# Kernel tuning notes

Hardware: AMD Instinct MI355X
Metric: run time of the kernel (lower is better)

The kernel has to match this reference:

```python
import jax, jax.numpy as jnp
import numpy as np

LN_EPS = 1e-5
NEG_SLOPE = 0.01  # torch LeakyReLU default
H, D = 16, 64


def _layernorm(x, g, b):
    m = jnp.mean(x, axis=-1, keepdims=True)
    v = jnp.var(x, axis=-1, keepdims=True)
    return (x - m) * jax.lax.rsqrt(v + LN_EPS) * g + b


def _mlp(x, ln_g, ln_b, W1, b1, W2, b2):
    h = _layernorm(x, ln_g, ln_b)
    h = jax.nn.gelu(h @ W1 + b1, approximate=False)
    return h @ W2 + b2


def _gather_nodes(node_msg, edge_index):
    # node_msg: (b,n,c), edge_index: (b,n,k) -> (b,n,k,c)
    return jax.vmap(lambda nm, ei: nm[ei])(node_msg, edge_index)


def setup_inputs() -> dict:
    key = jax.random.key(0)
    ks = jax.random.split(key, 16)
    b, n, k = 2, 1024, 32
    dim, pdim, msg_dim = 512, 256, 256
    s = 0.02
    inp = {
        'node_repr': jax.random.normal(ks[0], (b, n, dim), jnp.float32),
        'edge_repr': jax.random.normal(ks[1], (b, n, k, pdim), jnp.float32),
        'edge_index': jax.random.randint(ks[2], (b, n, k), 0, n, jnp.int32),
        'edge_mask': jax.random.randint(ks[3], (b, n, k), 0, 2, jnp.int32),
        'mask_bw': jnp.ones((b, n, k, 1), jnp.float32),
        'W_edge_msg': s * jax.random.normal(ks[4], (pdim, msg_dim), jnp.float32),
        'W_node_src': s * jax.random.normal(ks[5], (dim, msg_dim), jnp.float32),
        'W_node_tgt': s * jax.random.normal(ks[6], (dim, msg_dim), jnp.float32),
        'msg_ln_g': jnp.ones((msg_dim,), jnp.float32),
        'msg_ln_b': jnp.zeros((msg_dim,), jnp.float32),
        'msg_W1': s * jax.random.normal(ks[7], (msg_dim, 4 * msg_dim), jnp.float32),
        'msg_b1': jnp.zeros((4 * msg_dim,), jnp.float32),
        'msg_W2': s * jax.random.normal(ks[8], (4 * msg_dim, msg_dim), jnp.float32),
        'msg_b2': jnp.zeros((msg_dim,), jnp.float32),
        'W_gate': jnp.zeros((dim, msg_dim), jnp.float32),   # init_weights: zeros
        'b_gate': -jnp.ones((msg_dim,), jnp.float32),       # init_weights: -1
        'W_out': s * jax.random.normal(ks[9], (msg_dim, dim), jnp.float32),
        'W_msg': s * jax.random.normal(ks[10], (msg_dim, msg_dim), jnp.float32),
        'W_attn_bias': s * jax.random.normal(ks[11], (msg_dim, H), jnp.float32),
        'W_gat_value': s * jax.random.normal(ks[12], (msg_dim, H * D), jnp.float32),
        'W_gat_gate': jnp.zeros((dim, H * D), jnp.float32),
        'b_gat_gate': -jnp.ones((H * D,), jnp.float32),
        'W_gat_out': s * jax.random.normal(ks[13], (H * D, dim), jnp.float32),
        'node_ln_g': jnp.ones((dim,), jnp.float32),
        'node_ln_b': jnp.zeros((dim,), jnp.float32),
        'node_W1': s * jax.random.normal(ks[14], (dim, 4 * dim), jnp.float32),
        'node_b1': jnp.zeros((4 * dim,), jnp.float32),
        'node_W2': s * jax.random.normal(ks[15], (4 * dim, dim), jnp.float32),
        'node_b2': jnp.zeros((dim,), jnp.float32),
    }
    return inp


def reference(node_repr, edge_repr, edge_index, edge_mask, mask_bw,
              W_edge_msg, W_node_src, W_node_tgt,
              msg_ln_g, msg_ln_b, msg_W1, msg_b1, msg_W2, msg_b2,
              W_gate, b_gate, W_out,
              W_msg, W_attn_bias, W_gat_value, W_gat_gate, b_gat_gate, W_gat_out,
              node_ln_g, node_ln_b, node_W1, node_b1, node_W2, node_b2):
    b, n, k = edge_index.shape
    em_bool = edge_mask.astype(bool)          # (b,n,k)
    em_f = edge_mask.astype(node_repr.dtype)

    # edge-wise message: edge proj + gathered src node proj + broadcast tgt node proj
    node_msg = node_repr @ W_node_src                      # (b,n,msg)
    msg = edge_repr @ W_edge_msg \
        + _gather_nodes(node_msg, edge_index) * mask_bw \
        + (node_repr @ W_node_tgt)[:, :, None, :]          # (b,n,k,msg)
    msg = _mlp(msg, msg_ln_g, msg_ln_b, msg_W1, msg_b1, msg_W2, msg_b2)
    msg = jnp.where(em_bool[..., None], msg, 0.0)

    # global (mean-pooled, gated) path
    o = (msg * em_f[..., None]).sum(-2) / (em_f.sum(-1, keepdims=True) + 1e-6)
    o = jax.nn.sigmoid(node_repr @ W_gate + b_gate) * o
    dh = o @ W_out                                         # (b,n,dim)

    # GAT path: per-node attention over its k neighbors
    ab = jnp.where(NEG_SLOPE < 1, jax.nn.leaky_relu(msg @ W_msg, NEG_SLOPE), msg) @ W_attn_bias  # (b,n,k,H)
    ab = jnp.where(em_bool[..., None], ab, -jnp.finfo(ab.dtype).max)
    attn = jax.nn.softmax(ab, axis=2)                      # softmax over k
    v = (msg @ W_gat_value).reshape(b, n, k, H, D)
    og = jnp.einsum('bnkh,bnkhd->bnhd', attn, v).reshape(b, n, H * D)
    og = jax.nn.sigmoid(node_repr @ W_gat_gate + b_gat_gate) * og
    dh = dh + og @ W_gat_out

    # residual + node MLP (dropout is identity in eval mode)
    node_repr = node_repr + dh
    node_repr = node_repr + _mlp(node_repr, node_ln_g, node_ln_b, node_W1, node_b1, node_W2, node_b2)
    return node_repr
```

## Files before the change

kernel.cpp:

```cpp
#include <hip/hip_runtime.h>
#include <hip/hip_bf16.h>

typedef unsigned short u16;
typedef short s16x8 __attribute__((ext_vector_type(8)));
typedef float f32x4 __attribute__((ext_vector_type(4)));
typedef float f32x8 __attribute__((ext_vector_type(8)));
typedef u16 u16x8 __attribute__((ext_vector_type(8)));

#define DEV static __device__ __forceinline__

DEV float b2f(u16 u){ unsigned int i=((unsigned int)u)<<16; float f; __builtin_memcpy(&f,&i,4); return f; }
DEV u16 f2b(float x){ __hip_bfloat16 h=__float2bfloat16(x); u16 u; __builtin_memcpy(&u,&h,2); return u; }
DEV f32x4 MFMA(s16x8 a, s16x8 b, f32x4 c){ return __builtin_amdgcn_mfma_f32_16x16x32_bf16(a,b,c,0,0,0); }
DEV s16x8 LD8(const u16* p){ return *(const s16x8*)p; }
DEV s16x8 cvt8(const float* p){
  s16x8 r;
  #pragma unroll
  for (int i=0;i<8;i++) r[i] = (short)f2b(p[i]);
  return r;
}
DEV float geluf(float x){ return 0.5f*x*(1.0f+erff(x*0.70710678118654752f)); }
DEV float sigmf(float x){ return 1.0f/(1.0f+__expf(-x)); }

DEV void gload16(const u16* g, u16* l){
  __builtin_amdgcn_global_load_lds((const __attribute__((address_space(1))) void*)g,
                                   (__attribute__((address_space(3))) void*)l, 16, 0, 0);
}

#define WS_WeT   0
#define WS_W1T   65536
#define WS_W2T   327680
#define WS_WmT   589824
#define WS_WvT   655360
#define WS_WoT   917504
#define WS_WgoT  1048576
#define WS_nW1T  1572864
#define WS_nW2T  2621440
#define WS_SrcT  3670016
#define WS_TgtT  3801088
#define WS_GateT 3932160
#define WS_GgT   4063232
#define WS_NM    4587520
#define WS_TGT   5111808
#define WS_GP    5636096
#define WS_GG    6160384
#define WS_MSG   8257536
#define WS_U2    8257536
#define WS_X     10354688
#define WS_Y     12451840
#define WS_WM    25034752
#define WS_U1    33423360
#define WS_YE    33947648
#define WS_H     50724864

struct P13 { const float* p[13]; };
__device__ const int TR_START[14] = {0,16,80,144,160,224,256,384,640,896,928,960,992,1120};
__device__ const int TR_R[13]   = {256,256,1024,256,256,256,1024,512,2048,512,512,512,512};
__device__ const int TR_C[13]   = {256,1024,256,256,1024,512,512,2048,512,256,256,256,1024};
__device__ const int TR_DST[13] = {WS_WeT,WS_W1T,WS_W2T,WS_WmT,WS_WvT,WS_WoT,WS_WgoT,
                                   WS_nW1T,WS_nW2T,WS_SrcT,WS_TgtT,WS_GateT,WS_GgT};

__global__ __launch_bounds__(256) void k_transpose(P13 ps, u16* __restrict__ ws){
  __shared__ alignas(16) u16 Ts[64][72];
  const int t = threadIdx.x;
  int bid = blockIdx.x;
  int mi = 0;
  #pragma unroll 1
  while (bid >= TR_START[mi+1]) ++mi;
  const float* src = ps.p[mi];
  const int R = TR_R[mi], C = TR_C[mi];
  u16* dst = ws + TR_DST[mi];
  const int ti = bid - TR_START[mi];
  const int tcn = C >> 6;
  const int tr = ti / tcn, tc = ti % tcn;
  {
    const int row = t >> 2, cs = (t & 3) * 16;
    const float* sp = src + (tr*64 + row)*C + tc*64 + cs;
    u16x8 a, b;
    #pragma unroll
    for (int i=0;i<8;i++){ a[i]=f2b(sp[i]); b[i]=f2b(sp[8+i]); }
    *(u16x8*)&Ts[row][cs]   = a;
    *(u16x8*)&Ts[row][cs+8] = b;
  }
  __syncthreads();
  {
    const int col = t >> 2, rs = (t & 3) * 16;
    u16x8 a, b;
    #pragma unroll
    for (int i=0;i<8;i++){ a[i]=Ts[rs+i][col]; b[i]=Ts[rs+8+i][col]; }
    u16* dp = dst + (tc*64 + col)*R + tr*64 + rs;
    *(u16x8*)dp = a;
    *(u16x8*)(dp+8) = b;
  }
}

__global__ __launch_bounds__(256) void k_proj(const float* __restrict__ node_repr,
                                              const float* __restrict__ bgate,
                                              const float* __restrict__ bgg,
                                              u16* __restrict__ ws){
  const int t=threadIdx.x, lid=t&63, w=t>>6, g=lid>>4, q=lid&15;
  const int rb = blockIdx.x, yb = blockIdx.y;
  const u16* BT; u16* dst; int Nseg, colbase, act=0; const float* bias=nullptr;
  if (yb < 4){ BT=ws+WS_SrcT;  dst=ws+WS_NM; Nseg=256;  colbase=yb*64; }
  else if (yb < 8){ BT=ws+WS_TgtT;  dst=ws+WS_TGT; Nseg=256; colbase=(yb-4)*64; }
  else if (yb < 12){ BT=ws+WS_GateT; dst=ws+WS_GP; Nseg=256; colbase=(yb-8)*64; act=1; bias=bgate; }
  else { BT=ws+WS_GgT; dst=ws+WS_GG; Nseg=1024; colbase=(yb-12)*64; act=1; bias=bgg; }
  const int wr=(w>>1)*32, wcl=(w&1)*32;
  f32x4 acc[2][2] = {};
  for (int kk=0; kk<512; kk+=32){
    s16x8 af[2], bfr[2];
    #pragma unroll
    for (int i=0;i<2;i++) af[i] = cvt8(node_repr + (rb*64 + wr + i*16 + q)*512 + kk + 8*g);
    #pragma unroll
    for (int j=0;j<2;j++) bfr[j] = LD8(BT + (colbase + wcl + j*16 + q)*512 + kk + 8*g);
    #pragma unroll
    for (int i=0;i<2;i++)
      #pragma unroll
      for (int j=0;j<2;j++) acc[i][j] = MFMA(af[i], bfr[j], acc[i][j]);
  }
  #pragma unroll
  for (int i=0;i<2;i++)
    #pragma unroll
    for (int j=0;j<2;j++)
      #pragma unroll
      for (int r=0;r<4;r++){
        const int row = rb*64 + wr + i*16 + g*4 + r;
        const int col = wcl + j*16 + q;
        float v = acc[i][j][r];
        if (act) v = sigmf(v + bias[colbase+col]);
        dst[row*Nseg + colbase + col] = f2b(v);
      }
}

#define GB_S 528
__global__ __launch_bounds__(256) void k_edgepre(
    const float* __restrict__ edge_repr, const int* __restrict__ edge_index,
    const float* __restrict__ mask_bw,
    const float* __restrict__ ln_g, const float* __restrict__ ln_b,
    u16* __restrict__ ws)
{
  __shared__ alignas(16) char Gb[64*GB_S];
  __shared__ alignas(16) u16 As[64*32];
  __shared__ alignas(16) u16 Bs[256*32];
  __shared__ float rsS[4][64], rsQ[4][64];
  __shared__ int idxL[64]; __shared__ float mbwL[64];

  const int t=threadIdx.x, lid=t&63, w=t>>6, g=lid>>4, q=lid&15;
  const int R0 = blockIdx.x * 64;
  const int wc = w * 64;

  if (t < 64){
    idxL[t] = edge_index[R0+t];
    mbwL[t] = mask_bw[R0+t];
  }
  __syncthreads();

  const u16* nm = ws + WS_NM;
  const u16* tg = ws + WS_TGT;

  #pragma unroll
  for (int it=0; it<8; ++it){
    const int v = t + 256*it;
    const int row = v >> 5;
    const int sc  = (v & 31) * 8;
    const int er  = R0 + row;
    const int gnd = er >> 5;
    const int bi  = gnd >> 10;
    const int srow = bi*1024 + idxL[row];
    const float mb = mbwL[row];
    u16x8 nv = *(const u16x8*)(nm + srow*256 + sc);
    u16x8 tv = *(const u16x8*)(tg + gnd*256 + sc);
    u16x8 ov;
    #pragma unroll
    for (int j2=0;j2<8;j2++) ov[j2] = f2b(b2f(nv[j2])*mb + b2f(tv[j2]));
    *(u16x8*)(Gb + row*GB_S + 2*sc) = ov;
  }
  __syncthreads();

  f32x4 acc[4][4];
  #pragma unroll
  for (int i=0;i<4;i++)
    #pragma unroll
    for (int r=0;r<4;r++){
      const int row = i*16 + g*4 + r;
      #pragma unroll
      for (int j=0;j<4;j++){
        const int col = wc + j*16 + q;
        acc[i][j][r] = b2f(*(const u16*)(Gb + row*GB_S + 2*col));
      }
    }
  for (int kk=0; kk<256; kk+=32){
    __syncthreads();
    {
      const int row = t >> 2, c0 = (t & 3) * 8;
      const float* sp = edge_repr + (R0 + row)*256 + kk + c0;
      u16x8 av;
      #pragma unroll
      for (int j2=0;j2<8;j2++) av[j2] = f2b(sp[j2]);
      *(u16x8*)(As + row*32 + c0) = av;
    }
    #pragma unroll
    for (int j=0;j<4;j++){
      const int s = t + 256*j;
      const int brow = s >> 2, ko = (s & 3) * 8;
      u16* ldsB = Bs + (w*64 + 256*j)*8;
      gload16(ws + WS_WeT + brow*256 + kk + ko, ldsB);
    }
    __syncthreads();
    s16x8 af[4], bfr[4];
    #pragma unroll
    for (int i=0;i<4;i++) af[i]  = *(const s16x8*)(As + (i*16+q)*32 + g*8);
    #pragma unroll
    for (int j=0;j<4;j++) bfr[j] = *(const s16x8*)(Bs + (wc + j*16 + q)*32 + g*8);
    #pragma unroll
    for (int i=0;i<4;i++)
      #pragma unroll
      for (int j=0;j<4;j++) acc[i][j] = MFMA(af[i], bfr[j], acc[i][j]);
  }
  #pragma unroll
  for (int i=0;i<4;i++)
    #pragma unroll
    for (int r=0;r<4;r++){
      float s=0.f, s2=0.f;
      #pragma unroll
      for (int j=0;j<4;j++){ float v=acc[i][j][r]; s+=v; s2+=v*v; }
      #pragma unroll
      for (int m=1;m<16;m<<=1){ s += __shfl_xor(s,m,64); s2 += __shfl_xor(s2,m,64); }
      if (q==0){ const int row=i*16+g*4+r; rsS[w][row]=s; rsQ[w][row]=s2; }
    }
  __syncthreads();
  u16* Ye = ws + WS_YE;
  #pragma unroll
  for (int i=0;i<4;i++)
    #pragma unroll
    for (int r=0;r<4;r++){
      const int row=i*16+g*4+r;
      const float s  = rsS[0][row]+rsS[1][row]+rsS[2][row]+rsS[3][row];
      const float s2 = rsQ[0][row]+rsQ[1][row]+rsQ[2][row]+rsQ[3][row];
      const float mean = s*(1.f/256.f);
      const float var  = s2*(1.f/256.f) - mean*mean;
      const float rstd = rsqrtf(var + 1e-5f);
      #pragma unroll
      for (int j=0;j<4;j++){
        const int col = wc + j*16 + q;
        Ye[(R0+row)*256 + col] = f2b((acc[i][j][r]-mean)*rstd*ln_g[col] + ln_b[col]);
      }
    }
}

__global__ __launch_bounds__(256) void k_mlp1(const u16* __restrict__ A,
                                              const u16* __restrict__ BT,
                                              const float* __restrict__ b1,
                                              u16* __restrict__ H){
  __shared__ alignas(16) u16 As[128*32];
  __shared__ alignas(16) u16 Bs[128*32];
  const int t=threadIdx.x, lid=t&63, w=t>>6, g=lid>>4, q=lid&15;
  const int r0 = blockIdx.x*128, n0 = blockIdx.y*128;
  const int wr=(w>>1)*64, wc2=(w&1)*64;
  f32x4 acc[4][4] = {};
  for (int kk=0;kk<256;kk+=32){
    __syncthreads();
    #pragma unroll
    for (int j=0;j<2;j++){
      const int v = t + 256*j;
      const int row = v>>2, sg = (v&3)*8;
      u16* ldsA = As + (w*64 + 256*j)*8;
      u16* ldsB = Bs + (w*64 + 256*j)*8;
      gload16(A  + (r0+row)*256 + kk + sg, ldsA);
      gload16(BT + (n0+row)*256 + kk + sg, ldsB);
    }
    __syncthreads();
    s16x8 af[4], bf_[4];
    #pragma unroll
    for (int i=0;i<4;i++) af[i]  = *(const s16x8*)(As + (wr+i*16+q)*32 + g*8);
    #pragma unroll
    for (int j=0;j<4;j++) bf_[j] = *(const s16x8*)(Bs + (wc2+j*16+q)*32 + g*8);
    #pragma unroll
    for (int i=0;i<4;i++)
      #pragma unroll
      for (int j=0;j<4;j++) acc[i][j] = MFMA(af[i], bf_[j], acc[i][j]);
  }
  #pragma unroll
  for (int i=0;i<4;i++)
    #pragma unroll
    for (int j=0;j<4;j++)
      #pragma unroll
      for (int r=0;r<4;r++){
        const int row = r0 + wr + i*16 + g*4 + r;
        const int col = n0 + wc2 + j*16 + q;
        H[row*1024 + col] = f2b(geluf(acc[i][j][r] + b1[col]));
      }
}

__global__ __launch_bounds__(256) void k_mlp2(const u16* __restrict__ A,
                                              const u16* __restrict__ BT,
                                              const float* __restrict__ b2,
                                              const int* __restrict__ em,
                                              u16* __restrict__ msg){
  __shared__ alignas(16) u16 As[128*32];
  __shared__ alignas(16) u16 Bs[128*32];
  __shared__ int emL[128];
  const int t=threadIdx.x, lid=t&63, w=t>>6, g=lid>>4, q=lid&15;
  const int r0 = blockIdx.x*128, n0 = blockIdx.y*128;
  const int wr=(w>>1)*64, wc2=(w&1)*64;
  if (t < 128) emL[t] = em[r0 + t];
  f32x4 acc[4][4] = {};
  for (int kk=0;kk<1024;kk+=32){
    __syncthreads();
    #pragma unroll
    for (int j=0;j<2;j++){
      const int v = t + 256*j;
      const int row = v>>2, sg = (v&3)*8;
      u16* ldsA = As + (w*64 + 256*j)*8;
      u16* ldsB = Bs + (w*64 + 256*j)*8;
      gload16(A  + (r0+row)*1024 + kk + sg, ldsA);
      gload16(BT + (n0+row)*1024 + kk + sg, ldsB);
    }
    __syncthreads();
    s16x8 af[4], bf_[4];
    #pragma unroll
    for (int i=0;i<4;i++) af[i]  = *(const s16x8*)(As + (wr+i*16+q)*32 + g*8);
    #pragma unroll
    for (int j=0;j<4;j++) bf_[j] = *(const s16x8*)(Bs + (wc2+j*16+q)*32 + g*8);
    #pragma unroll
    for (int i=0;i<4;i++)
      #pragma unroll
      for (int j=0;j<4;j++) acc[i][j] = MFMA(af[i], bf_[j], acc[i][j]);
  }
  #pragma unroll
  for (int i=0;i<4;i++)
    #pragma unroll
    for (int j=0;j<4;j++)
      #pragma unroll
      for (int r=0;r<4;r++){
        const int rl  = wr + i*16 + g*4 + r;
        const int col = n0 + wc2 + j*16 + q;
        float v = acc[i][j][r] + b2[col];
        if (!emL[rl]) v = 0.f;
        msg[(r0+rl)*256 + col] = f2b(v);
      }
}

__global__ __launch_bounds__(256) void k_tm(const u16* __restrict__ A,
                                            const u16* __restrict__ BT,
                                            u16* __restrict__ Tm){
  __shared__ alignas(16) u16 As[128*32];
  __shared__ alignas(16) u16 Bs[128*32];
  const int t=threadIdx.x, lid=t&63, w=t>>6, g=lid>>4, q=lid&15;
  const int r0 = blockIdx.x*128, n0 = blockIdx.y*128;
  const int wr=(w>>1)*64, wc2=(w&1)*64;
  f32x4 acc[4][4] = {};
  for (int kk=0;kk<256;kk+=32){
    __syncthreads();
    #pragma unroll
    for (int j=0;j<2;j++){
      const int v = t + 256*j;
      const int row = v>>2, sg = (v&3)*8;
      u16* ldsA = As + (w*64 + 256*j)*8;
      u16* ldsB = Bs + (w*64 + 256*j)*8;
      gload16(A  + (r0+row)*256 + kk + sg, ldsA);
      gload16(BT + (n0+row)*256 + kk + sg, ldsB);
    }
    __syncthreads();
    s16x8 af[4], bf_[4];
    #pragma unroll
    for (int i=0;i<4;i++) af[i]  = *(const s16x8*)(As + (wr+i*16+q)*32 + g*8);
    #pragma unroll
    for (int j=0;j<4;j++) bf_[j] = *(const s16x8*)(Bs + (wc2+j*16+q)*32 + g*8);
    #pragma unroll
    for (int i=0;i<4;i++)
      #pragma unroll
      for (int j=0;j<4;j++) acc[i][j] = MFMA(af[i], bf_[j], acc[i][j]);
  }
  #pragma unroll
  for (int i=0;i<4;i++)
    #pragma unroll
    for (int j=0;j<4;j++)
      #pragma unroll
      for (int r=0;r<4;r++){
        const int row = r0 + wr + i*16 + g*4 + r;
        const int col = n0 + wc2 + j*16 + q;
        float v = acc[i][j][r];
        Tm[row*256 + col] = f2b(v > 0.f ? v : 0.01f*v);
      }
}

__global__ __launch_bounds__(256) void k_ab(const u16* __restrict__ A,
                                            const float* __restrict__ Wab,
                                            float* __restrict__ AB){
  __shared__ alignas(16) u16 As[128*32];
  __shared__ alignas(16) char WbT[16*528];
  const int t=threadIdx.x, lid=t&63, w=t>>6, g=lid>>4, q=lid&15;
  const int r0 = blockIdx.x*128;
  {
    const float* wr_ = Wab + t*16;
    #pragma unroll
    for (int h=0;h<16;h++) *(u16*)(WbT + h*528 + 2*t) = f2b(wr_[h]);
  }
  f32x4 acc[2] = {};
  for (int kk=0;kk<256;kk+=32){
    __syncthreads();
    #pragma unroll
    for (int j=0;j<2;j++){
      const int s = t + 256*j;
      const int row = s>>2, ko = (s&3)*8;
      u16* ldsA = As + (w*64 + 256*j)*8;
      gload16(A + (r0+row)*256 + kk + ko, ldsA);
    }
    __syncthreads();
    s16x8 bf_ = *(const s16x8*)(WbT + q*528 + 2*(kk + 8*g));
    #pragma unroll
    for (int i=0;i<2;i++){
      s16x8 af = *(const s16x8*)(As + (w*32 + i*16 + q)*32 + g*8);
      acc[i] = MFMA(af, bf_, acc[i]);
    }
  }
  #pragma unroll
  for (int i=0;i<2;i++)
    #pragma unroll
    for (int r=0;r<4;r++){
      const int row = r0 + w*32 + i*16 + g*4 + r;
      AB[row*16 + q] = acc[i][r];
    }
}

#define AM_S 528
#define MT_S 80
__global__ __launch_bounds__(256) void k_attn2(const int* __restrict__ edge_mask,
                                               u16* __restrict__ ws){
  __shared__ alignas(16) char Am[32*AM_S];
  __shared__ alignas(16) char Mt[256*MT_S];
  __shared__ alignas(16) char Pb[16*80];
  __shared__ float Pp[32][16];
  __shared__ int emL[32];
  __shared__ float cntS;

  const int t=threadIdx.x, lid=t&63, w=t>>6, g=lid>>4, q=lid&15;
  const int nd = blockIdx.x;
  const int wc = w*64;
  const u16* msg = ws + WS_MSG + nd*32*256;
  const float* ab = (const float*)(ws + WS_YE) + nd*32*16;

  if (t < 32) emL[t] = edge_mask[nd*32 + t];
  #pragma unroll
  for (int it=0; it<4; ++it){
    const int v = t + 256*it;
    const int row = v >> 5, sc = (v & 31)*8;
    u16x8 val = *(const u16x8*)(msg + row*256 + sc);
    *(u16x8*)(Am + row*AM_S + 2*sc) = val;
  }
  {
    const int k = t >> 4, h = t & 15;
    Pp[k][h]    = ab[k*16 + h];
    Pp[k+16][h] = ab[(k+16)*16 + h];
  }
  __syncthreads();
  if (t == 0){ float c=0.f; for (int k=0;k<32;k++) c += emL[k]?1.f:0.f; cntS=c; }
  {
    const int c = t;
    #pragma unroll 1
    for (int k=0;k<32;k++){
      u16 vv = *(const u16*)(Am + k*AM_S + 2*c);
      *(u16*)(Mt + c*MT_S + 2*k) = vv;
    }
  }
  if (t < 16){
    const int h = t;
    float m = -3.4028235e38f;
    float pv[32];
    for (int k=0;k<32;k++){ pv[k] = emL[k] ? Pp[k][h] : -3.4028235e38f; m = fmaxf(m, pv[k]); }
    float s = 0.f;
    float ev[32];
    for (int k=0;k<32;k++){ ev[k]=__expf(pv[k]-m); s+=ev[k]; }
    const float inv = 1.f/s;
    for (int k=0;k<32;k++) *(u16*)(Pb + h*80 + 2*k) = f2b(ev[k]*inv);
  }
  __syncthreads();
  {
    s16x8 pa = *(const s16x8*)(Pb + q*80 + 2*(8*g));
    f32x4 wmac[4] = {};
    #pragma unroll
    for (int j=0;j<4;j++){
      s16x8 mb = *(const s16x8*)(Mt + (wc + j*16 + q)*MT_S + 2*(8*g));
      wmac[j] = MFMA(pa, mb, wmac[j]);
    }
    u16* wmw = ws + WS_WM;
    #pragma unroll
    for (int j=0;j<4;j++)
      #pragma unroll
      for (int r=0;r<4;r++){
        const int hh = g*4 + r;
        const int col = wc + j*16 + q;
        wmw[hh*(2048*256) + nd*256 + col] = f2b(wmac[j][r]);
      }
  }
  {
    const int c = t;
    float s = 0.f;
    #pragma unroll 1
    for (int k=0;k<32;k++) s += b2f(*(const u16*)(Am + k*AM_S + 2*c));
    const float o = s / (cntS + 1e-6f);
    ws[WS_U1 + nd*256 + c] = f2b(o * b2f(ws[WS_GP + nd*256 + c]));
  }
}

__global__ __launch_bounds__(256) void k_og(u16* __restrict__ ws){
  const int t=threadIdx.x, lid=t&63, w=t>>6, g=lid>>4, q=lid&15;
  const int rb=blockIdx.x, h=blockIdx.y;
  const int wr=(w>>1)*32, wcl=(w&1)*32;
  const u16* A  = ws + WS_WM  + h*(2048*256);
  const u16* BT = ws + WS_WvT;
  f32x4 acc[2][2] = {};
  for (int kk=0;kk<256;kk+=32){
    s16x8 af[2], bfr[2];
    #pragma unroll
    for (int i=0;i<2;i++) af[i] = LD8(A + (rb*64 + wr + i*16 + q)*256 + kk + 8*g);
    #pragma unroll
    for (int j=0;j<2;j++) bfr[j] = LD8(BT + (h*64 + wcl + j*16 + q)*256 + kk + 8*g);
    #pragma unroll
    for (int i=0;i<2;i++)
      #pragma unroll
      for (int j=0;j<2;j++) acc[i][j] = MFMA(af[i], bfr[j], acc[i][j]);
  }
  #pragma unroll
  for (int i=0;i<2;i++)
    #pragma unroll
    for (int j=0;j<2;j++)
      #pragma unroll
      for (int r=0;r<4;r++){
        const int row = rb*64 + wr + i*16 + g*4 + r;
        const int col = h*64 + wcl + j*16 + q;
        const float gv = b2f(ws[WS_GG + row*1024 + col]);
        ws[WS_U2 + row*1024 + col] = f2b(acc[i][j][r] * gv);
      }
}

__global__ __launch_bounds__(256) void k_dh(const float* __restrict__ node_repr, u16* __restrict__ ws){
  const int t=threadIdx.x, lid=t&63, w=t>>6, g=lid>>4, q=lid&15;
  const int rb=blockIdx.x, cb=blockIdx.y*64;
  const int wr=(w>>1)*32, wcl=(w&1)*32;
  float* Xf = (float*)(ws + WS_X);
  f32x4 acc[2][2] = {};
  for (int kk=0;kk<256;kk+=32){
    s16x8 af[2], bfr[2];
    #pragma unroll
    for (int i=0;i<2;i++) af[i] = LD8(ws + WS_U1 + (rb*64 + wr + i*16 + q)*256 + kk + 8*g);
    #pragma unroll
    for (int j=0;j<2;j++) bfr[j] = LD8(ws + WS_WoT + (cb + wcl + j*16 + q)*256 + kk + 8*g);
    #pragma unroll
    for (int i=0;i<2;i++)
      #pragma unroll
      for (int j=0;j<2;j++) acc[i][j] = MFMA(af[i], bfr[j], acc[i][j]);
  }
  for (int kk=0;kk<1024;kk+=32){
    s16x8 af[2], bfr[2];
    #pragma unroll
    for (int i=0;i<2;i++) af[i] = LD8(ws + WS_U2 + (rb*64 + wr + i*16 + q)*1024 + kk + 8*g);
    #pragma unroll
    for (int j=0;j<2;j++) bfr[j] = LD8(ws + WS_WgoT + (cb + wcl + j*16 + q)*1024 + kk + 8*g);
    #pragma unroll
    for (int i=0;i<2;i++)
      #pragma unroll
      for (int j=0;j<2;j++) acc[i][j] = MFMA(af[i], bfr[j], acc[i][j]);
  }
  #pragma unroll
  for (int i=0;i<2;i++)
    #pragma unroll
    for (int j=0;j<2;j++)
      #pragma unroll
      for (int r=0;r<4;r++){
        const int row = rb*64 + wr + i*16 + g*4 + r;
        const int col = cb + wcl + j*16 + q;
        Xf[row*512 + col] = acc[i][j][r] + node_repr[row*512 + col];
      }
}

__global__ __launch_bounds__(256) void k_ln512(const float* __restrict__ g_, const float* __restrict__ b_,
                                               u16* __restrict__ ws){
  const int t=threadIdx.x, wid=t>>6, lane=t&63;
  const int row = blockIdx.x*4 + wid;
  const float* xr = (const float*)(ws + WS_X) + row*512;
  f32x8 xv = *(const f32x8*)(xr + lane*8);
  float s=0.f, s2=0.f;
  #pragma unroll
  for (int i=0;i<8;i++){ s+=xv[i]; s2+=xv[i]*xv[i]; }
  #pragma unroll
  for (int m=1;m<64;m<<=1){ s += __shfl_xor(s,m,64); s2 += __shfl_xor(s2,m,64); }
  const float mean = s*(1.f/512.f);
  const float var  = s2*(1.f/512.f) - mean*mean;
  const float rstd = rsqrtf(var + 1e-5f);
  u16x8 yv;
  #pragma unroll
  for (int i=0;i<8;i++) yv[i] = f2b((xv[i]-mean)*rstd*g_[lane*8+i] + b_[lane*8+i]);
  *(u16x8*)(ws + WS_Y + row*512 + lane*8) = yv;
}

__global__ __launch_bounds__(256) void k_nmlp1(const u16* __restrict__ A,
                                               const u16* __restrict__ BT,
                                               const float* __restrict__ b1,
                                               u16* __restrict__ H){
  __shared__ alignas(16) u16 As[128*32];
  __shared__ alignas(16) u16 Bs[128*32];
  const int t=threadIdx.x, lid=t&63, w=t>>6, g=lid>>4, q=lid&15;
  const int r0 = blockIdx.x*128, n0 = blockIdx.y*128;
  const int wr=(w>>1)*64, wc2=(w&1)*64;
  f32x4 acc[4][4] = {};
  for (int kk=0;kk<512;kk+=32){
    __syncthreads();
    #pragma unroll
    for (int j=0;j<2;j++){
      const int v = t + 256*j;
      const int row = v>>2, sg = (v&3)*8;
      u16* ldsA = As + (w*64 + 256*j)*8;
      u16* ldsB = Bs + (w*64 + 256*j)*8;
      gload16(A  + (r0+row)*512 + kk + sg, ldsA);
      gload16(BT + (n0+row)*512 + kk + sg, ldsB);
    }
    __syncthreads();
    s16x8 af[4], bf_[4];
    #pragma unroll
    for (int i=0;i<4;i++) af[i]  = *(const s16x8*)(As + (wr+i*16+q)*32 + g*8);
    #pragma unroll
    for (int j=0;j<4;j++) bf_[j] = *(const s16x8*)(Bs + (wc2+j*16+q)*32 + g*8);
    #pragma unroll
    for (int i=0;i<4;i++)
      #pragma unroll
      for (int j=0;j<4;j++) acc[i][j] = MFMA(af[i], bf_[j], acc[i][j]);
  }
  #pragma unroll
  for (int i=0;i<4;i++)
    #pragma unroll
    for (int j=0;j<4;j++)
      #pragma unroll
      for (int r=0;r<4;r++){
        const int row = r0 + wr + i*16 + g*4 + r;
        const int col = n0 + wc2 + j*16 + q;
        H[row*2048 + col] = f2b(geluf(acc[i][j][r] + b1[col]));
      }
}

__global__ __launch_bounds__(256) void k_nmlp2(const u16* __restrict__ A,
                                               const u16* __restrict__ BT,
                                               const float* __restrict__ b2,
                                               const float* __restrict__ Xf,
                                               float* __restrict__ out){
  __shared__ alignas(16) u16 As[64*32];
  __shared__ alignas(16) u16 Bs[64*32];
  const int t=threadIdx.x, lid=t&63, w=t>>6, g=lid>>4, q=lid&15;
  const int r0 = blockIdx.x*64, n0 = blockIdx.y*64;
  const int wr=(w>>1)*32, wc2=(w&1)*32;
  f32x4 acc[2][2] = {};
  for (int kk=0;kk<2048;kk+=32){
    __syncthreads();
    {
      const int row = t>>2, sg = (t&3)*8;
      u16* ldsA = As + (w*64)*8;
      u16* ldsB = Bs + (w*64)*8;
      gload16(A  + (r0+row)*2048 + kk + sg, ldsA);
      gload16(BT + (n0+row)*2048 + kk + sg, ldsB);
    }
    __syncthreads();
    s16x8 af[2], bf_[2];
    #pragma unroll
    for (int i=0;i<2;i++) af[i]  = *(const s16x8*)(As + (wr+i*16+q)*32 + g*8);
    #pragma unroll
    for (int j=0;j<2;j++) bf_[j] = *(const s16x8*)(Bs + (wc2+j*16+q)*32 + g*8);
    #pragma unroll
    for (int i=0;i<2;i++)
      #pragma unroll
      for (int j=0;j<2;j++) acc[i][j] = MFMA(af[i], bf_[j], acc[i][j]);
  }
  #pragma unroll
  for (int i=0;i<2;i++)
    #pragma unroll
    for (int j=0;j<2;j++)
      #pragma unroll
      for (int r=0;r<4;r++){
        const int row = r0 + wr + i*16 + g*4 + r;
        const int col = n0 + wc2 + j*16 + q;
        out[row*512 + col] = acc[i][j][r] + b2[col] + Xf[row*512 + col];
      }
}

extern "C" void kernel_launch(void* const* d_in, const int* in_sizes, int n_in,
                              void* d_out, int out_size, void* d_ws, size_t ws_size,
                              hipStream_t stream){
  (void)in_sizes; (void)n_in; (void)out_size; (void)ws_size;
  const float* node_repr = (const float*)d_in[0];
  const float* edge_repr = (const float*)d_in[1];
  const int* edge_index = (const int*)d_in[2];
  const int* edge_mask  = (const int*)d_in[3];
  const float* mask_bw = (const float*)d_in[4];
  u16* ws = (u16*)d_ws;

  P13 ps;
  const int srcIdx[13] = {5,10,12,17,19,16,22,25,27,6,7,14,20};
  for (int i=0;i<13;i++) ps.p[i] = (const float*)d_in[srcIdx[i]];

  hipLaunchKernelGGL(k_transpose, dim3(1120), dim3(256), 0, stream, ps, ws);
  hipLaunchKernelGGL(k_proj, dim3(32,28), dim3(256), 0, stream,
                     node_repr, (const float*)d_in[15], (const float*)d_in[21], ws);
  hipLaunchKernelGGL(k_edgepre, dim3(1024), dim3(256), 0, stream,
                     edge_repr, edge_index, mask_bw,
                     (const float*)d_in[8], (const float*)d_in[9], ws);
  for (int grp=0; grp<2; ++grp){
    const u16* Ag = ws + WS_YE + grp*32768*256;
    u16* Hg = ws + WS_H;
    u16* msgg = ws + WS_MSG + grp*32768*256;
    const int* emg = edge_mask + grp*32768;
    hipLaunchKernelGGL(k_mlp1, dim3(256,8), dim3(256), 0, stream,
                       Ag, ws + WS_W1T, (const float*)d_in[11], Hg);
    hipLaunchKernelGGL(k_mlp2, dim3(256,2), dim3(256), 0, stream,
                       Hg, ws + WS_W2T, (const float*)d_in[13], emg, msgg);
  }
  hipLaunchKernelGGL(k_tm, dim3(512,2), dim3(256), 0, stream,
                     ws + WS_MSG, ws + WS_WmT, ws + WS_H);
  hipLaunchKernelGGL(k_ab, dim3(512), dim3(256), 0, stream,
                     ws + WS_H, (const float*)d_in[18], (float*)(ws + WS_YE));
  hipLaunchKernelGGL(k_attn2, dim3(2048), dim3(256), 0, stream,
                     edge_mask, ws);
  hipLaunchKernelGGL(k_og, dim3(32,16), dim3(256), 0, stream, ws);
  hipLaunchKernelGGL(k_dh, dim3(32,8), dim3(256), 0, stream, node_repr, ws);
  hipLaunchKernelGGL(k_ln512, dim3(512), dim3(256), 0, stream,
                     (const float*)d_in[23], (const float*)d_in[24], ws);
  hipLaunchKernelGGL(k_nmlp1, dim3(16,16), dim3(256), 0, stream,
                     ws + WS_Y, ws + WS_nW1T, (const float*)d_in[26], ws + WS_H);
  hipLaunchKernelGGL(k_nmlp2, dim3(32,8), dim3(256), 0, stream,
                     ws + WS_H, ws + WS_nW2T, (const float*)d_in[28],
                     (const float*)(ws + WS_X), (float*)d_out);
}
```

Before: 357.4 us.

## Use tanh GELU, alias LDS in edge prologue, stage k_dh operands through LDS

Replaces the exact erf-based GELU in both MLP first-layer epilogues with a tanh approximation built on __expf, cutting transcendental cost. In k_edgepre the edge GEMM now runs first and the gathered node term is added afterwards, which lets the gather buffer and the A/B tiles share one LDS allocation and lowers LDS use, possibly raising occupancy. k_dh now stages its A and B tiles through LDS with global_load_lds instead of reading them directly from global memory per lane. The tanh GELU is an approximation that deviates slightly from the reference's exact GELU.

```diff
diff --git a/kernel.cpp b/kernel.cpp
--- a/kernel.cpp
+++ b/kernel.cpp
@@ -19,7 +19,12 @@
   for (int i=0;i<8;i++) r[i] = (short)f2b(p[i]);
   return r;
 }
-DEV float geluf(float x){ return 0.5f*x*(1.0f+erff(x*0.70710678118654752f)); }
+DEV float gelu_fast(float x){
+  float u = 0.7978845608f*(x + 0.044715f*x*x*x);
+  float e = __expf(2.f*u);
+  float th = 1.f - 2.f/(e + 1.f);
+  return 0.5f*x*(1.f + th);
+}
 DEV float sigmf(float x){ return 1.0f/(1.0f+__expf(-x)); }
 
 DEV void gload16(const u16* g, u16* l){
@@ -139,25 +144,54 @@
     const float* __restrict__ ln_g, const float* __restrict__ ln_b,
     u16* __restrict__ ws)
 {
-  __shared__ alignas(16) char Gb[64*GB_S];
-  __shared__ alignas(16) u16 As[64*32];
-  __shared__ alignas(16) u16 Bs[256*32];
+  __shared__ alignas(16) char SH[64*GB_S];
   __shared__ float rsS[4][64], rsQ[4][64];
   __shared__ int idxL[64]; __shared__ float mbwL[64];
 
   const int t=threadIdx.x, lid=t&63, w=t>>6, g=lid>>4, q=lid&15;
   const int R0 = blockIdx.x * 64;
   const int wc = w * 64;
+  u16* As = (u16*)SH;
+  u16* Bs = (u16*)(SH + 4096);
 
   if (t < 64){
     idxL[t] = edge_index[R0+t];
     mbwL[t] = mask_bw[R0+t];
   }
+
+  f32x4 acc[4][4] = {};
+  for (int kk=0; kk<256; kk+=32){
+    __syncthreads();
+    {
+      const int row = t >> 2, c0 = (t & 3) * 8;
+      const float* sp = edge_repr + (R0 + row)*256 + kk + c0;
+      u16x8 av;
+      #pragma unroll
+      for (int j2=0;j2<8;j2++) av[j2] = f2b(sp[j2]);
+      *(u16x8*)(As + row*32 + c0) = av;
+    }
+    #pragma unroll
+    for (int j=0;j<4;j++){
+      const int s = t + 256*j;
+      const int brow = s >> 2, ko = (s & 3) * 8;
+      u16* ldsB = Bs + (w*64 + 256*j)*8;
+      gload16(ws + WS_WeT + brow*256 + kk + ko, ldsB);
+    }
+    __syncthreads();
+    s16x8 af[4], bfr[4];
+    #pragma unroll
+    for (int i=0;i<4;i++) af[i]  = *(const s16x8*)(As + (i*16+q)*32 + g*8);
+    #pragma unroll
+    for (int j=0;j<4;j++) bfr[j] = *(const s16x8*)(Bs + (wc + j*16 + q)*32 + g*8);
+    #pragma unroll
+    for (int i=0;i<4;i++)
+      #pragma unroll
+      for (int j=0;j<4;j++) acc[i][j] = MFMA(af[i], bfr[j], acc[i][j]);
+  }
   __syncthreads();
 
   const u16* nm = ws + WS_NM;
   const u16* tg = ws + WS_TGT;
-
   #pragma unroll
   for (int it=0; it<8; ++it){
     const int v = t + 256*it;
@@ -173,11 +207,9 @@
     u16x8 ov;
     #pragma unroll
     for (int j2=0;j2<8;j2++) ov[j2] = f2b(b2f(nv[j2])*mb + b2f(tv[j2]));
-    *(u16x8*)(Gb + row*GB_S + 2*sc) = ov;
+    *(u16x8*)(SH + row*GB_S + 2*sc) = ov;
   }
   __syncthreads();
-
-  f32x4 acc[4][4];
   #pragma unroll
   for (int i=0;i<4;i++)
     #pragma unroll
@@ -186,37 +218,9 @@
       #pragma unroll
       for (int j=0;j<4;j++){
         const int col = wc + j*16 + q;
-        acc[i][j][r] = b2f(*(const u16*)(Gb + row*GB_S + 2*col));
-      }
-    }
-  for (int kk=0; kk<256; kk+=32){
-    __syncthreads();
-    {
-      const int row = t >> 2, c0 = (t & 3) * 8;
-      const float* sp = edge_repr + (R0 + row)*256 + kk + c0;
-      u16x8 av;
-      #pragma unroll
-      for (int j2=0;j2<8;j2++) av[j2] = f2b(sp[j2]);
-      *(u16x8*)(As + row*32 + c0) = av;
-    }
-    #pragma unroll
-    for (int j=0;j<4;j++){
-      const int s = t + 256*j;
-      const int brow = s >> 2, ko = (s & 3) * 8;
-      u16* ldsB = Bs + (w*64 + 256*j)*8;
-      gload16(ws + WS_WeT + brow*256 + kk + ko, ldsB);
-    }
-    __syncthreads();
-    s16x8 af[4], bfr[4];
-    #pragma unroll
-    for (int i=0;i<4;i++) af[i]  = *(const s16x8*)(As + (i*16+q)*32 + g*8);
-    #pragma unroll
-    for (int j=0;j<4;j++) bfr[j] = *(const s16x8*)(Bs + (wc + j*16 + q)*32 + g*8);
-    #pragma unroll
-    for (int i=0;i<4;i++)
-      #pragma unroll
-      for (int j=0;j<4;j++) acc[i][j] = MFMA(af[i], bfr[j], acc[i][j]);
-  }
+        acc[i][j][r] += b2f(*(const u16*)(SH + row*GB_S + 2*col));
+      }
+    }
   #pragma unroll
   for (int i=0;i<4;i++)
     #pragma unroll
@@ -288,7 +292,7 @@
       for (int r=0;r<4;r++){
         const int row = r0 + wr + i*16 + g*4 + r;
         const int col = n0 + wc2 + j*16 + q;
-        H[row*1024 + col] = f2b(geluf(acc[i][j][r] + b1[col]));
+        H[row*1024 + col] = f2b(gelu_fast(acc[i][j][r] + b1[col]));
       }
 }
 
@@ -536,32 +540,48 @@
 }
 
 __global__ __launch_bounds__(256) void k_dh(const float* __restrict__ node_repr, u16* __restrict__ ws){
+  __shared__ alignas(16) u16 As[64*32];
+  __shared__ alignas(16) u16 Bs[64*32];
   const int t=threadIdx.x, lid=t&63, w=t>>6, g=lid>>4, q=lid&15;
   const int rb=blockIdx.x, cb=blockIdx.y*64;
-  const int wr=(w>>1)*32, wcl=(w&1)*32;
+  const int wr=(w>>1)*32, wc2=(w&1)*32;
   float* Xf = (float*)(ws + WS_X);
   f32x4 acc[2][2] = {};
   for (int kk=0;kk<256;kk+=32){
-    s16x8 af[2], bfr[2];
-    #pragma unroll
-    for (int i=0;i<2;i++) af[i] = LD8(ws + WS_U1 + (rb*64 + wr + i*16 + q)*256 + kk + 8*g);
-    #pragma unroll
-    for (int j=0;j<2;j++) bfr[j] = LD8(ws + WS_WoT + (cb + wcl + j*16 + q)*256 + kk + 8*g);
+    __syncthreads();
+    {
+      const int row = t>>2, sg = (t&3)*8;
+      gload16(ws + WS_U1  + (rb*64+row)*256 + kk + sg, As + (w*64)*8);
+      gload16(ws + WS_WoT + (cb+row)*256    + kk + sg, Bs + (w*64)*8);
+    }
+    __syncthreads();
+    s16x8 af[2], bf_[2];
+    #pragma unroll
+    for (int i=0;i<2;i++) af[i]  = *(const s16x8*)(As + (wr+i*16+q)*32 + g*8);
+    #pragma unroll
+    for (int j=0;j<2;j++) bf_[j] = *(const s16x8*)(Bs + (wc2+j*16+q)*32 + g*8);
     #pragma unroll
     for (int i=0;i<2;i++)
       #pragma unroll
-      for (int j=0;j<2;j++) acc[i][j] = MFMA(af[i], bfr[j], acc[i][j]);
+      for (int j=0;j<2;j++) acc[i][j] = MFMA(af[i], bf_[j], acc[i][j]);
   }
   for (int kk=0;kk<1024;kk+=32){
-    s16x8 af[2], bfr[2];
-    #pragma unroll
-    for (int i=0;i<2;i++) af[i] = LD8(ws + WS_U2 + (rb*64 + wr + i*16 + q)*1024 + kk + 8*g);
-    #pragma unroll
-    for (int j=0;j<2;j++) bfr[j] = LD8(ws + WS_WgoT + (cb + wcl + j*16 + q)*1024 + kk + 8*g);
+    __syncthreads();
+    {
+      const int row = t>>2, sg = (t&3)*8;
+      gload16(ws + WS_U2   + (rb*64+row)*1024 + kk + sg, As + (w*64)*8);
+      gload16(ws + WS_WgoT + (cb+row)*1024    + kk + sg, Bs + (w*64)*8);
+    }
+    __syncthreads();
+    s16x8 af[2], bf_[2];
+    #pragma unroll
+    for (int i=0;i<2;i++) af[i]  = *(const s16x8*)(As + (wr+i*16+q)*32 + g*8);
+    #pragma unroll
+    for (int j=0;j<2;j++) bf_[j] = *(const s16x8*)(Bs + (wc2+j*16+q)*32 + g*8);
     #pragma unroll
     for (int i=0;i<2;i++)
       #pragma unroll
-      for (int j=0;j<2;j++) acc[i][j] = MFMA(af[i], bfr[j], acc[i][j]);
+      for (int j=0;j<2;j++) acc[i][j] = MFMA(af[i], bf_[j], acc[i][j]);
   }
   #pragma unroll
   for (int i=0;i<2;i++)
@@ -570,7 +590,7 @@
       #pragma unroll
       for (int r=0;r<4;r++){
         const int row = rb*64 + wr + i*16 + g*4 + r;
-        const int col = cb + wcl + j*16 + q;
+        const int col = cb + wc2 + j*16 + q;
         Xf[row*512 + col] = acc[i][j][r] + node_repr[row*512 + col];
       }
 }
@@ -635,7 +655,7 @@
       for (int r=0;r<4;r++){
         const int row = r0 + wr + i*16 + g*4 + r;
         const int col = n0 + wc2 + j*16 + q;
-        H[row*2048 + col] = f2b(geluf(acc[i][j][r] + b1[col]));
+        H[row*2048 + col] = f2b(gelu_fast(acc[i][j][r] + b1[col]));
       }
 }
 
@@ -654,10 +674,8 @@
     __syncthreads();
     {
       const int row = t>>2, sg = (t&3)*8;
-      u16* ldsA = As + (w*64)*8;
-      u16* ldsB = Bs + (w*64)*8;
-      gload16(A  + (r0+row)*2048 + kk + sg, ldsA);
-      gload16(BT + (n0+row)*2048 + kk + sg, ldsB);
+      gload16(A  + (r0+row)*2048 + kk + sg, As + (w*64)*8);
+      gload16(BT + (n0+row)*2048 + kk + sg, Bs + (w*64)*8);
     }
     __syncthreads();
     s16x8 af[2], bf_[2];
```

Result: slower. 370.7 us (+3.7%).

## Use tanh GELU, pre-convert node_repr to bf16, vectorize loads, alias edgepre LDS

Applied to the files above, without the earlier changes.

Replaces the exact erf GELU in both MLP hidden epilogues with a tanh approximation built on __expf. Adds a kernel that converts node_repr to bf16 once, so k_proj loads bf16 fragments instead of converting fp32 on every K step. Vectorizes the edge_repr fp32 loads in k_edgepre and makes its A/B staging buffers share the gather buffer, cutting LDS use to raise occupancy. The tanh GELU changes numerics slightly, and there is one more kernel launch.

```diff
diff --git a/kernel.cpp b/kernel.cpp
--- a/kernel.cpp
+++ b/kernel.cpp
@@ -13,13 +13,12 @@
 DEV u16 f2b(float x){ __hip_bfloat16 h=__float2bfloat16(x); u16 u; __builtin_memcpy(&u,&h,2); return u; }
 DEV f32x4 MFMA(s16x8 a, s16x8 b, f32x4 c){ return __builtin_amdgcn_mfma_f32_16x16x32_bf16(a,b,c,0,0,0); }
 DEV s16x8 LD8(const u16* p){ return *(const s16x8*)p; }
-DEV s16x8 cvt8(const float* p){
-  s16x8 r;
-  #pragma unroll
-  for (int i=0;i<8;i++) r[i] = (short)f2b(p[i]);
-  return r;
-}
-DEV float geluf(float x){ return 0.5f*x*(1.0f+erff(x*0.70710678118654752f)); }
+DEV float gelu_fast(float x){
+  float u = 0.7978845608f*(x + 0.044715f*x*x*x);
+  float e = __expf(2.f*u);
+  float th = 1.f - 2.f/(e + 1.f);
+  return 0.5f*x*(1.f + th);
+}
 DEV float sigmf(float x){ return 1.0f/(1.0f+__expf(-x)); }
 
 DEV void gload16(const u16* g, u16* l){
@@ -94,12 +93,21 @@
   }
 }
 
-__global__ __launch_bounds__(256) void k_proj(const float* __restrict__ node_repr,
-                                              const float* __restrict__ bgate,
+__global__ __launch_bounds__(256) void k_cvtnode(const float* __restrict__ src, u16* __restrict__ dst){
+  const int i = (blockIdx.x*256 + threadIdx.x)*8;
+  f32x8 v = *(const f32x8*)(src + i);
+  u16x8 o;
+  #pragma unroll
+  for (int j=0;j<8;j++) o[j] = f2b(v[j]);
+  *(u16x8*)(dst + i) = o;
+}
+
+__global__ __launch_bounds__(256) void k_proj(const float* __restrict__ bgate,
                                               const float* __restrict__ bgg,
                                               u16* __restrict__ ws){
   const int t=threadIdx.x, lid=t&63, w=t>>6, g=lid>>4, q=lid&15;
   const int rb = blockIdx.x, yb = blockIdx.y;
+  const u16* nb = ws + WS_H;
   const u16* BT; u16* dst; int Nseg, colbase, act=0; const float* bias=nullptr;
   if (yb < 4){ BT=ws+WS_SrcT;  dst=ws+WS_NM; Nseg=256;  colbase=yb*64; }
   else if (yb < 8){ BT=ws+WS_TgtT;  dst=ws+WS_TGT; Nseg=256; colbase=(yb-4)*64; }
@@ -110,7 +118,7 @@
   for (int kk=0; kk<512; kk+=32){
     s16x8 af[2], bfr[2];
     #pragma unroll
-    for (int i=0;i<2;i++) af[i] = cvt8(node_repr + (rb*64 + wr + i*16 + q)*512 + kk + 8*g);
+    for (int i=0;i<2;i++) af[i] = LD8(nb + (rb*64 + wr + i*16 + q)*512 + kk + 8*g);
     #pragma unroll
     for (int j=0;j<2;j++) bfr[j] = LD8(BT + (colbase + wcl + j*16 + q)*512 + kk + 8*g);
     #pragma unroll
@@ -139,15 +147,15 @@
     const float* __restrict__ ln_g, const float* __restrict__ ln_b,
     u16* __restrict__ ws)
 {
-  __shared__ alignas(16) char Gb[64*GB_S];
-  __shared__ alignas(16) u16 As[64*32];
-  __shared__ alignas(16) u16 Bs[256*32];
+  __shared__ alignas(16) char SH[64*GB_S];
   __shared__ float rsS[4][64], rsQ[4][64];
   __shared__ int idxL[64]; __shared__ float mbwL[64];
 
   const int t=threadIdx.x, lid=t&63, w=t>>6, g=lid>>4, q=lid&15;
   const int R0 = blockIdx.x * 64;
   const int wc = w * 64;
+  u16* As = (u16*)SH;
+  u16* Bs = (u16*)(SH + 4096);
 
   if (t < 64){
     idxL[t] = edge_index[R0+t];
@@ -157,7 +165,6 @@
 
   const u16* nm = ws + WS_NM;
   const u16* tg = ws + WS_TGT;
-
   #pragma unroll
   for (int it=0; it<8; ++it){
     const int v = t + 256*it;
@@ -173,10 +180,9 @@
     u16x8 ov;
     #pragma unroll
     for (int j2=0;j2<8;j2++) ov[j2] = f2b(b2f(nv[j2])*mb + b2f(tv[j2]));
-    *(u16x8*)(Gb + row*GB_S + 2*sc) = ov;
+    *(u16x8*)(SH + row*GB_S + 2*sc) = ov;
   }
   __syncthreads();
-
   f32x4 acc[4][4];
   #pragma unroll
   for (int i=0;i<4;i++)
@@ -186,7 +192,7 @@
       #pragma unroll
       for (int j=0;j<4;j++){
         const int col = wc + j*16 + q;
-        acc[i][j][r] = b2f(*(const u16*)(Gb + row*GB_S + 2*col));
+        acc[i][j][r] = b2f(*(const u16*)(SH + row*GB_S + 2*col));
       }
     }
   for (int kk=0; kk<256; kk+=32){
@@ -194,9 +200,10 @@
     {
       const int row = t >> 2, c0 = (t & 3) * 8;
       const float* sp = edge_repr + (R0 + row)*256 + kk + c0;
+      f32x8 fv = *(const f32x8*)sp;
       u16x8 av;
       #pragma unroll
-      for (int j2=0;j2<8;j2++) av[j2] = f2b(sp[j2]);
+      for (int j2=0;j2<8;j2++) av[j2] = f2b(fv[j2]);
       *(u16x8*)(As + row*32 + c0) = av;
     }
     #pragma unroll
@@ -288,7 +295,7 @@
       for (int r=0;r<4;r++){
         const int row = r0 + wr + i*16 + g*4 + r;
         const int col = n0 + wc2 + j*16 + q;
-        H[row*1024 + col] = f2b(geluf(acc[i][j][r] + b1[col]));
+        H[row*1024 + col] = f2b(gelu_fast(acc[i][j][r] + b1[col]));
       }
 }
 
@@ -635,7 +642,7 @@
       for (int r=0;r<4;r++){
         const int row = r0 + wr + i*16 + g*4 + r;
         const int col = n0 + wc2 + j*16 + q;
-        H[row*2048 + col] = f2b(geluf(acc[i][j][r] + b1[col]));
+        H[row*2048 + col] = f2b(gelu_fast(acc[i][j][r] + b1[col]));
       }
 }
 
@@ -654,10 +661,8 @@
     __syncthreads();
     {
       const int row = t>>2, sg = (t&3)*8;
-      u16* ldsA = As + (w*64)*8;
-      u16* ldsB = Bs + (w*64)*8;
-      gload16(A  + (r0+row)*2048 + kk + sg, ldsA);
-      gload16(BT + (n0+row)*2048 + kk + sg, ldsB);
+      gload16(A  + (r0+row)*2048 + kk + sg, As + (w*64)*8);
+      gload16(BT + (n0+row)*2048 + kk + sg, Bs + (w*64)*8);
     }
     __syncthreads();
     s16x8 af[2], bf_[2];
@@ -698,8 +703,9 @@
   for (int i=0;i<13;i++) ps.p[i] = (const float*)d_in[srcIdx[i]];
 
   hipLaunchKernelGGL(k_transpose, dim3(1120), dim3(256), 0, stream, ps, ws);
+  hipLaunchKernelGGL(k_cvtnode, dim3(512), dim3(256), 0, stream, node_repr, ws + WS_H);
   hipLaunchKernelGGL(k_proj, dim3(32,28), dim3(256), 0, stream,
-                     node_repr, (const float*)d_in[15], (const float*)d_in[21], ws);
+                     (const float*)d_in[15], (const float*)d_in[21], ws);
   hipLaunchKernelGGL(k_edgepre, dim3(1024), dim3(256), 0, stream,
                      edge_repr, edge_index, mask_bw,
                      (const float*)d_in[8], (const float*)d_in[9], ws);
```

Result: no change. 358.4 us (+0.3%).
